# Kernel optimization log

Hardware: AMD Instinct MI355X
Metric: run time of the kernel (lower is better)

The kernel has to match this reference:

```python
import jax, jax.numpy as jnp
import numpy as np

DIM = 2048
N_HEADS = 16
HEAD_DIM = 128
KV_HEADS = 1
ROPE_BASE = 10000.0


def _rope_tables(T, dim, dtype):
    inv_freq = 1.0 / (ROPE_BASE ** (jnp.arange(0, dim, 2, dtype=jnp.float32) / dim))
    t = jnp.arange(T, dtype=jnp.float32)
    freqs = jnp.einsum('i,j->ij', t, inv_freq)          # [T, dim/2]
    emb = jnp.concatenate([freqs, freqs], axis=-1)      # [T, dim]
    cos = jnp.cos(emb)[None, None, :, :].astype(dtype)  # [1,1,T,dim]
    sin = jnp.sin(emb)[None, None, :, :].astype(dtype)
    return cos, sin


def _rotate_half(x):
    x1, x2 = jnp.split(x, 2, axis=-1)
    return jnp.concatenate([-x2, x1], axis=-1)


def setup_inputs() -> dict:
    key = jax.random.key(0)
    k1, k2, k3, k4, k5 = jax.random.split(key, 5)
    B, T = 2, 2048
    x = jax.random.normal(k1, (B, T, DIM), dtype=jnp.float32)
    # additive causal mask: 0 on/below diagonal, -1e9 above
    causal = jnp.triu(jnp.full((T, T), -1e9, dtype=jnp.float32), k=1)
    attn_mask = causal[None, None, :, :]
    s = 1.0 / np.sqrt(DIM)
    wq = jax.random.normal(k2, (DIM, N_HEADS * HEAD_DIM), dtype=jnp.float32) * s
    wk = jax.random.normal(k3, (DIM, KV_HEADS * HEAD_DIM), dtype=jnp.float32) * s
    wv = jax.random.normal(k4, (DIM, KV_HEADS * HEAD_DIM), dtype=jnp.float32) * s
    wo = jax.random.normal(k5, (N_HEADS * HEAD_DIM, DIM), dtype=jnp.float32) * s
    return {"x": x, "attn_mask": attn_mask, "wq": wq, "wk": wk, "wv": wv, "wo": wo}


def reference(x, attn_mask, wq, wk, wv, wo):
    B, T, C = x.shape
    q = (x @ wq).reshape(B, T, N_HEADS, HEAD_DIM).transpose(0, 2, 1, 3)   # [B,H,T,d]
    k = (x @ wk).reshape(B, T, KV_HEADS, HEAD_DIM).transpose(0, 2, 1, 3)  # [B,1,T,d]
    v = (x @ wv).reshape(B, T, KV_HEADS, HEAD_DIM).transpose(0, 2, 1, 3)  # [B,1,T,d]
    cos, sin = _rope_tables(T, HEAD_DIM, x.dtype)
    q = q * cos + _rotate_half(q) * sin
    k = k * cos + _rotate_half(k) * sin
    # KV head broadcasts over the H dim inside matmul (MQA expand path)
    att = jnp.matmul(q, k.swapaxes(-1, -2)) / np.sqrt(HEAD_DIM)          # [B,H,T,T]
    att = att + attn_mask
    w = jax.nn.softmax(att, axis=-1)
    y = jnp.matmul(w, v)                                                  # [B,H,T,d]
    y = y.transpose(0, 2, 1, 3).reshape(B, T, N_HEADS * HEAD_DIM)
    y = y @ wo
    k_exp = jnp.broadcast_to(k, (B, N_HEADS, T, HEAD_DIM))
    v_exp = jnp.broadcast_to(v, (B, N_HEADS, T, HEAD_DIM))
    return y, k_exp, v_exp
```

## Files before the change

kernel.cpp:

```cpp
#include <hip/hip_runtime.h>
#include <hip/hip_bf16.h>
#include <cstdint>
#include <cstddef>

#define B_SZ   2
#define T_SEQ  2048
#define C_DIM  2048
#define NH     16
#define HD     128

typedef __attribute__((ext_vector_type(8))) short s8v;
typedef __attribute__((ext_vector_type(4))) float f32x4;

typedef __attribute__((address_space(3))) char lds_char;
typedef __attribute__((address_space(1))) const char glob_char;

__device__ __forceinline__ unsigned short f2bf(float f) {
    union { float f; uint32_t i; } v; v.f = f;
    uint32_t r = (v.i + 0x7FFFu + ((v.i >> 16) & 1u)) >> 16;
    return (unsigned short)r;
}

__device__ __forceinline__ unsigned short cvt1_bf16(float f) {
    unsigned int w;
    asm("v_cvt_pk_bf16_f32 %0, %1, %2" : "=v"(w) : "v"(f), "v"(f));
    return (unsigned short)w;
}

template <int CTRL>
__device__ __forceinline__ float dpp_ror_f(float x) {
    int t = __builtin_amdgcn_update_dpp(__float_as_int(x), __float_as_int(x),
                                        CTRL, 0xf, 0xf, false);
    return __int_as_float(t);
}
__device__ __forceinline__ float rowmax16(float v) {
    v = fmaxf(v, dpp_ror_f<0x121>(v));
    v = fmaxf(v, dpp_ror_f<0x122>(v));
    v = fmaxf(v, dpp_ror_f<0x124>(v));
    v = fmaxf(v, dpp_ror_f<0x128>(v));
    return v;
}

__global__ void k_f32_to_bf16(const float* __restrict__ in,
                              unsigned short* __restrict__ out, int n4) {
    int i = blockIdx.x * blockDim.x + threadIdx.x;
    int stride = gridDim.x * blockDim.x;
    for (; i < n4; i += stride) {
        float4 v = reinterpret_cast<const float4*>(in)[i];
        ushort4 o;
        o.x = f2bf(v.x); o.y = f2bf(v.y); o.z = f2bf(v.z); o.w = f2bf(v.w);
        reinterpret_cast<ushort4*>(out)[i] = o;
    }
}

__global__ void k_transp_bf16(const float* __restrict__ in,
                              unsigned short* __restrict__ out,
                              int R, int C, int ldo) {
    __shared__ unsigned short tile[64][66];
    int x0 = blockIdx.x * 64, y0 = blockIdx.y * 64;
    int tx = threadIdx.x, ty = threadIdx.y;
#pragma unroll
    for (int j = 0; j < 16; ++j) {
        int r = y0 + ty + j * 4;
        tile[ty + j * 4][tx] = f2bf(in[(size_t)r * C + x0 + tx]);
    }
    __syncthreads();
#pragma unroll
    for (int j = 0; j < 16; ++j) {
        int orow = x0 + ty + j * 4;
        out[(size_t)orow * ldo + y0 + tx] = tile[tx][ty + j * 4];
    }
}

__global__ void k_rope_tab(float* __restrict__ cosT, float* __restrict__ sinT) {
    int idx = blockIdx.x * blockDim.x + threadIdx.x;
    if (idx >= T_SEQ * 64) return;
    int t = idx >> 6, i = idx & 63;
    float inv = powf(10000.0f, -(float)i / 64.0f);
    float ang = (float)t * inv;
    cosT[idx] = cosf(ang);
    sinT[idx] = sinf(ang);
}

#define BM 128
#define BN 128
#define BK 64

__global__ __launch_bounds__(256) void k_gemm_bt(
        const unsigned short* __restrict__ A,
        const unsigned short* __restrict__ Bt,
        float* __restrict__ C, int M, int N, int K, int ldc) {
    __shared__ char smem[BM * BK * 2 + BN * BK * 2];
    char* As = smem;
    char* Bs = smem + BM * BK * 2;
    int tid = threadIdx.x, lane = tid & 63, wid = tid >> 6;
    int m0 = blockIdx.y * BM, n0 = blockIdx.x * BN;
    int wr = wid >> 1, wc = wid & 1;

    f32x4 acc[4][4] = {};

    int srow = wid * 32 + (lane >> 3);
    int cp = lane & 7;

    for (int k0 = 0; k0 < K; k0 += BK) {
#pragma unroll
        for (int i = 0; i < 4; ++i) {
            int row = srow + i * 8;
            int c = cp ^ (row & 7);
            const unsigned short* ga = A + (size_t)(m0 + row) * K + k0 + c * 8;
            const unsigned short* gb = Bt + (size_t)(n0 + row) * K + k0 + c * 8;
            __builtin_amdgcn_global_load_lds((glob_char*)ga,
                (lds_char*)(As + wid * 4096 + i * 1024), 16, 0, 0);
            __builtin_amdgcn_global_load_lds((glob_char*)gb,
                (lds_char*)(Bs + wid * 4096 + i * 1024), 16, 0, 0);
        }
        __syncthreads();

#pragma unroll
        for (int kc = 0; kc < 2; ++kc) {
            s8v af[4], bfr[4];
#pragma unroll
            for (int mi = 0; mi < 4; ++mi) {
                int row = wr * 64 + mi * 16 + (lane & 15);
                int slot = (kc * 4 + (lane >> 4)) ^ (row & 7);
                af[mi] = *reinterpret_cast<const s8v*>(As + row * 128 + slot * 16);
            }
#pragma unroll
            for (int ni = 0; ni < 4; ++ni) {
                int row = wc * 64 + ni * 16 + (lane & 15);
                int slot = (kc * 4 + (lane >> 4)) ^ (row & 7);
                bfr[ni] = *reinterpret_cast<const s8v*>(Bs + row * 128 + slot * 16);
            }
#pragma unroll
            for (int mi = 0; mi < 4; ++mi)
#pragma unroll
                for (int ni = 0; ni < 4; ++ni)
                    acc[mi][ni] = __builtin_amdgcn_mfma_f32_16x16x32_bf16(
                        af[mi], bfr[ni], acc[mi][ni], 0, 0, 0);
        }
        __syncthreads();
    }

#pragma unroll
    for (int mi = 0; mi < 4; ++mi) {
        int row = m0 + wr * 64 + mi * 16 + ((lane >> 4) << 2);
#pragma unroll
        for (int ni = 0; ni < 4; ++ni) {
            int col = n0 + wc * 64 + ni * 16 + (lane & 15);
            float* cp2 = C + (size_t)row * ldc + col;
#pragma unroll
            for (int r = 0; r < 4; ++r)
                cp2[(size_t)r * ldc] = acc[mi][ni][r];
        }
    }
}

__global__ void k_qkv_transform(const float* __restrict__ qkv,
                                const float* __restrict__ cosT,
                                const float* __restrict__ sinT,
                                unsigned short* __restrict__ qB,
                                unsigned short* __restrict__ kB,
                                unsigned short* __restrict__ vT,
                                float* __restrict__ kexp,
                                float* __restrict__ vexp) {
    int bt = blockIdx.x;
    int b = bt >> 11, t = bt & 2047;
    int tid = threadIdx.x;
    const float* base = qkv + (size_t)bt * 2304;
    const float SCALE = 0.08838834764831845f * 1.4426950408889634f;

    for (int i = tid; i < 1024; i += 256) {
        int h = i >> 6, d = i & 63;
        float c = cosT[t * 64 + d], s = sinT[t * 64 + d];
        float q1 = base[h * 128 + d], q2 = base[h * 128 + d + 64];
        float o1 = (q1 * c - q2 * s) * SCALE;
        float o2 = (q2 * c + q1 * s) * SCALE;
        size_t qoff = ((size_t)(b * NH + h) * T_SEQ + t) * HD + d;
        qB[qoff] = f2bf(o1);
        qB[qoff + 64] = f2bf(o2);
    }
    if (tid < 64) {
        int d = tid;
        float c = cosT[t * 64 + d], s = sinT[t * 64 + d];
        float k1 = base[2048 + d], k2 = base[2048 + d + 64];
        float o1 = k1 * c - k2 * s;
        float o2 = k2 * c + k1 * s;
        size_t koff = ((size_t)b * T_SEQ + t) * HD + d;
        kB[koff] = f2bf(o1);
        kB[koff + 64] = f2bf(o2);
#pragma unroll
        for (int h = 0; h < NH; ++h) {
            size_t eoff = ((size_t)(b * NH + h) * T_SEQ + t) * HD + d;
            kexp[eoff] = o1;
            kexp[eoff + 64] = o2;
        }
    }
    if (tid >= 128) {
        int d = tid - 128;
        float v = base[2176 + d];
        vT[((size_t)b * HD + d) * T_SEQ + t] = f2bf(v);
#pragma unroll
        for (int h = 0; h < NH; ++h)
            vexp[((size_t)(b * NH + h) * T_SEQ + t) * HD + d] = v;
    }
}

__global__ __launch_bounds__(256, 2) void k_flash_attn(
        const unsigned short* __restrict__ qB,
        const unsigned short* __restrict__ kB,
        const unsigned short* __restrict__ vT,
        unsigned short* __restrict__ yattn) {
    __shared__ char smem[81920];
    int tid = threadIdx.x, lane = tid & 63, wvid = tid >> 6;
    int blk = blockIdx.x;
    int g = blk >> 5;
    int qt = (g < 8) ? (15 - 2 * g) : (2 * g - 16);
    int bh = blk & 31;
    int b = bh >> 4, h = bh & 15;
    int q0 = qt * 128 + wvid * 32;

    char* Ks0 = smem;
    char* Vs0 = smem + 32768;
    char* pbase = smem + 65536 + wvid * 4096;

    const unsigned short* kbB   = kB + (size_t)b * T_SEQ * HD;
    const unsigned short* vbase = vT + (size_t)b * HD * T_SEQ;

    const unsigned short* qbase = qB + ((size_t)(b * NH + h) * T_SEQ + q0) * HD;
    s8v aq[2][4];
#pragma unroll
    for (int rt = 0; rt < 2; ++rt)
#pragma unroll
        for (int kc = 0; kc < 4; ++kc) {
            int row = rt * 16 + (lane & 15);
            aq[rt][kc] = *reinterpret_cast<const s8v*>(
                qbase + (size_t)row * HD + kc * 32 + (lane >> 4) * 8);
        }

    float m_r[2][4], l_r[2][4];
#pragma unroll
    for (int rt = 0; rt < 2; ++rt)
#pragma unroll
        for (int r = 0; r < 4; ++r) { m_r[rt][r] = -3e38f; l_r[rt][r] = 0.f; }
    f32x4 o[2][8] = {};

    int NT = 2 * qt + 2;

    auto stage = [&](int buf, int t) {
        int kv0 = t * 64;
#pragma unroll
        for (int j = 0; j < 4; ++j) {
            int n = j * 256 + tid;
            int row = n >> 4, ch = n & 15;
            const unsigned short* src =
                kbB + (size_t)(kv0 + row) * HD + (ch ^ (row & 7)) * 8;
            __builtin_amdgcn_global_load_lds((glob_char*)src,
                (lds_char*)(Ks0 + buf * 16384 + j * 4096 + wvid * 1024), 16, 0, 0);
        }
#pragma unroll
        for (int j = 0; j < 4; ++j) {
            int n = j * 256 + tid;
            int row = n >> 3, ch = n & 7;
            const unsigned short* src =
                vbase + (size_t)row * T_SEQ + kv0 + (ch ^ (row & 7)) * 8;
            __builtin_amdgcn_global_load_lds((glob_char*)src,
                (lds_char*)(Vs0 + buf * 16384 + j * 4096 + wvid * 1024), 16, 0, 0);
        }
    };

    stage(0, 0);
    asm volatile("s_waitcnt vmcnt(0)" ::: "memory");
    __builtin_amdgcn_s_barrier();
    __builtin_amdgcn_sched_barrier(0);

    for (int t = 0; t < NT; ++t) {
        int cur = t & 1;
        if (t + 1 < NT) stage(cur ^ 1, t + 1);
        int kv0 = t * 64;
        const char* Kc = Ks0 + cur * 16384;
        const char* Vc = Vs0 + cur * 16384;

        f32x4 sfr[2][4] = {};
        __builtin_amdgcn_s_setprio(1);
#pragma unroll
        for (int kc = 0; kc < 4; ++kc) {
            s8v kf[4];
#pragma unroll
            for (int n = 0; n < 4; ++n) {
                int row = n * 16 + (lane & 15);
                int byte = row * 256 +
                    ((kc * 64 + (lane >> 4) * 16) ^ ((row & 7) << 4));
                kf[n] = *reinterpret_cast<const s8v*>(Kc + byte);
            }
#pragma unroll
            for (int rt = 0; rt < 2; ++rt)
#pragma unroll
                for (int n = 0; n < 4; ++n)
                    sfr[rt][n] = __builtin_amdgcn_mfma_f32_16x16x32_bf16(
                        aq[rt][kc], kf[n], sfr[rt][n], 0, 0, 0);
        }
        __builtin_amdgcn_s_setprio(0);

        if (kv0 + 63 > q0) {
#pragma unroll
            for (int rt = 0; rt < 2; ++rt)
#pragma unroll
                for (int n = 0; n < 4; ++n)
#pragma unroll
                    for (int r = 0; r < 4; ++r) {
                        int col = kv0 + n * 16 + (lane & 15);
                        int row = q0 + rt * 16 + ((lane >> 4) << 2) + r;
                        if (col > row) sfr[rt][n][r] = -1e9f;
                    }
        }

#pragma unroll
        for (int rt = 0; rt < 2; ++rt) {
            float pm[4];
#pragma unroll
            for (int r = 0; r < 4; ++r) {
                float v0 = fmaxf(fmaxf(sfr[rt][0][r], sfr[rt][1][r]),
                                 fmaxf(sfr[rt][2][r], sfr[rt][3][r]));
                pm[r] = rowmax16(v0);
            }
            int ok = (pm[0] <= m_r[rt][0] + 8.0f) &
                     (pm[1] <= m_r[rt][1] + 8.0f) &
                     (pm[2] <= m_r[rt][2] + 8.0f) &
                     (pm[3] <= m_r[rt][3] + 8.0f);
            if (!__all(ok)) {
#pragma unroll
                for (int r = 0; r < 4; ++r) {
                    float mn = fmaxf(m_r[rt][r], pm[r]);
                    float al = exp2f(m_r[rt][r] - mn);
                    l_r[rt][r] *= al;
#pragma unroll
                    for (int ds = 0; ds < 8; ++ds)
                        o[rt][ds][r] *= al;
                    m_r[rt][r] = mn;
                }
            }
#pragma unroll
            for (int n = 0; n < 4; ++n)
#pragma unroll
                for (int r = 0; r < 4; ++r) {
                    float p = exp2f(sfr[rt][n][r] - m_r[rt][r]);
                    sfr[rt][n][r] = p;
                    l_r[rt][r] += p;
                }
        }

#pragma unroll
        for (int rt = 0; rt < 2; ++rt)
#pragma unroll
            for (int n = 0; n < 4; ++n)
#pragma unroll
                for (int r = 0; r < 4; ++r) {
                    int rowl = rt * 16 + ((lane >> 4) << 2) + r;
                    int byte = rowl * 128 + (n * 16 + (lane & 15)) * 2;
                    byte ^= ((rowl & 7) << 4);
                    *reinterpret_cast<unsigned short*>(pbase + byte) =
                        cvt1_bf16(sfr[rt][n][r]);
                }
        asm volatile("s_waitcnt lgkmcnt(0)" ::: "memory");
        __builtin_amdgcn_sched_barrier(0);

        __builtin_amdgcn_s_setprio(1);
#pragma unroll
        for (int kc2 = 0; kc2 < 2; ++kc2) {
            s8v pa[2];
#pragma unroll
            for (int rt = 0; rt < 2; ++rt) {
                int rowl = rt * 16 + (lane & 15);
                int byte = rowl * 128 +
                    ((kc2 * 64 + (lane >> 4) * 16) ^ ((rowl & 7) << 4));
                pa[rt] = *reinterpret_cast<const s8v*>(pbase + byte);
            }
#pragma unroll
            for (int ds = 0; ds < 8; ++ds) {
                int vrow = ds * 16 + (lane & 15);
                int vbyte = vrow * 128 +
                    ((kc2 * 64 + (lane >> 4) * 16) ^ ((vrow & 7) << 4));
                s8v bv = *reinterpret_cast<const s8v*>(Vc + vbyte);
#pragma unroll
                for (int rt = 0; rt < 2; ++rt)
                    o[rt][ds] = __builtin_amdgcn_mfma_f32_16x16x32_bf16(
                        pa[rt], bv, o[rt][ds], 0, 0, 0);
            }
        }
        __builtin_amdgcn_s_setprio(0);

        asm volatile("s_waitcnt vmcnt(0) lgkmcnt(0)" ::: "memory");
        __builtin_amdgcn_s_barrier();
        __builtin_amdgcn_sched_barrier(0);
    }

#pragma unroll
    for (int rt = 0; rt < 2; ++rt) {
        float inv[4];
#pragma unroll
        for (int r = 0; r < 4; ++r) {
            float lv = l_r[rt][r];
#pragma unroll
            for (int off = 1; off < 16; off <<= 1)
                lv += __shfl_xor(lv, off);
            inv[r] = 1.0f / lv;
        }
#pragma unroll
        for (int ds = 0; ds < 8; ++ds)
#pragma unroll
            for (int r = 0; r < 4; ++r) {
                int row = q0 + rt * 16 + ((lane >> 4) << 2) + r;
                int col = h * HD + ds * 16 + (lane & 15);
                yattn[((size_t)b * T_SEQ + row) * C_DIM + col] =
                    cvt1_bf16(o[rt][ds][r] * inv[r]);
            }
    }
}

extern "C" void kernel_launch(void* const* d_in, const int* in_sizes, int n_in,
                              void* d_out, int out_size, void* d_ws, size_t ws_size,
                              hipStream_t stream) {
    const float* x  = (const float*)d_in[0];
    const float* wq = (const float*)d_in[2];
    const float* wk = (const float*)d_in[3];
    const float* wv = (const float*)d_in[4];
    const float* wo = (const float*)d_in[5];

    char* ws = (char*)d_ws;
    size_t off = 0;
    auto alloc = [&](size_t bytes) -> void* {
        void* p = ws + off;
        off += (bytes + 255) & ~(size_t)255;
        return p;
    };
    unsigned short* xb   = (unsigned short*)alloc((size_t)4096 * 2048 * 2);
    unsigned short* wT   = (unsigned short*)alloc((size_t)2304 * 2048 * 2);
    unsigned short* woT  = (unsigned short*)alloc((size_t)2048 * 2048 * 2);
    float*          qkv  = (float*)alloc((size_t)4096 * 2304 * 4);
    float*          cosT = (float*)alloc((size_t)2048 * 64 * 4);
    float*          sinT = (float*)alloc((size_t)2048 * 64 * 4);
    unsigned short* qB   = (unsigned short*)alloc((size_t)2 * 16 * 2048 * 128 * 2);
    unsigned short* kB   = (unsigned short*)alloc((size_t)2 * 2048 * 128 * 2);
    unsigned short* vT   = (unsigned short*)alloc((size_t)2 * 128 * 2048 * 2);
    unsigned short* yattn = (unsigned short*)qkv;

    float* y_out = (float*)d_out;
    float* kexp  = y_out + (size_t)2 * 2048 * 2048;
    float* vexp  = kexp + (size_t)2 * 16 * 2048 * 128;

    dim3 tb(64, 4);
    k_f32_to_bf16<<<2048, 256, 0, stream>>>(x, xb, 4096 * 2048 / 4);
    k_transp_bf16<<<dim3(32, 32), tb, 0, stream>>>(wq, wT, 2048, 2048, 2048);
    k_transp_bf16<<<dim3(2, 32), tb, 0, stream>>>(wk, wT + (size_t)2048 * 2048, 2048, 128, 2048);
    k_transp_bf16<<<dim3(2, 32), tb, 0, stream>>>(wv, wT + (size_t)2176 * 2048, 2048, 128, 2048);
    k_transp_bf16<<<dim3(32, 32), tb, 0, stream>>>(wo, woT, 2048, 2048, 2048);
    k_rope_tab<<<512, 256, 0, stream>>>(cosT, sinT);

    k_gemm_bt<<<dim3(2304 / BN, 4096 / BM), 256, 0, stream>>>(
        xb, wT, qkv, 4096, 2304, 2048, 2304);
    k_qkv_transform<<<4096, 256, 0, stream>>>(qkv, cosT, sinT, qB, kB, vT, kexp, vexp);
    k_flash_attn<<<512, 256, 0, stream>>>(qB, kB, vT, yattn);
    k_gemm_bt<<<dim3(2048 / BN, 4096 / BM), 256, 0, stream>>>(
        yattn, woT, y_out, 4096, 2048, 2048, 2048);
}
```

Before: 253.8 us.

## Pair mirrored 64-row query tiles per block for balanced causal attention work

Measured after the change: 252.5 us. No clear change (-0.5%).

```diff
diff --git a/kernel.cpp b/kernel.cpp
--- a/kernel.cpp
+++ b/kernel.cpp
@@ -213,11 +213,15 @@
     __shared__ char smem[81920];
     int tid = threadIdx.x, lane = tid & 63, wvid = tid >> 6;
     int blk = blockIdx.x;
-    int g = blk >> 5;
-    int qt = (g < 8) ? (15 - 2 * g) : (2 * g - 16);
-    int bh = blk & 31;
-    int b = bh >> 4, h = bh & 15;
-    int q0 = qt * 128 + wvid * 32;
+    int b = blk >> 8;
+    int rem = blk & 255;
+    int h = rem & 15;
+    int jj = rem >> 4;
+    int j0 = 16 + jj;
+    int j1 = 15 - jj;
+    int qrow0[2];
+    qrow0[0] = j0 * 64 + wvid * 16;
+    qrow0[1] = j1 * 64 + wvid * 16;
 
     char* Ks0 = smem;
     char* Vs0 = smem + 32768;
@@ -226,16 +230,16 @@
     const unsigned short* kbB   = kB + (size_t)b * T_SEQ * HD;
     const unsigned short* vbase = vT + (size_t)b * HD * T_SEQ;
 
-    const unsigned short* qbase = qB + ((size_t)(b * NH + h) * T_SEQ + q0) * HD;
     s8v aq[2][4];
 #pragma unroll
-    for (int rt = 0; rt < 2; ++rt)
-#pragma unroll
-        for (int kc = 0; kc < 4; ++kc) {
-            int row = rt * 16 + (lane & 15);
+    for (int rt = 0; rt < 2; ++rt) {
+        const unsigned short* qbase =
+            qB + ((size_t)(b * NH + h) * T_SEQ + qrow0[rt]) * HD;
+#pragma unroll
+        for (int kc = 0; kc < 4; ++kc)
             aq[rt][kc] = *reinterpret_cast<const s8v*>(
-                qbase + (size_t)row * HD + kc * 32 + (lane >> 4) * 8);
-        }
+                qbase + (size_t)(lane & 15) * HD + kc * 32 + (lane >> 4) * 8);
+    }
 
     float m_r[2][4], l_r[2][4];
 #pragma unroll
@@ -244,7 +248,7 @@
         for (int r = 0; r < 4; ++r) { m_r[rt][r] = -3e38f; l_r[rt][r] = 0.f; }
     f32x4 o[2][8] = {};
 
-    int NT = 2 * qt + 2;
+    int NT = j0 + 1;
 
     auto stage = [&](int buf, int t) {
         int kv0 = t * 64;
@@ -279,6 +283,7 @@
         int kv0 = t * 64;
         const char* Kc = Ks0 + cur * 16384;
         const char* Vc = Vs0 + cur * 16384;
+        int act1 = (t <= j1);
 
         f32x4 sfr[2][4] = {};
         __builtin_amdgcn_s_setprio(1);
@@ -293,29 +298,31 @@
                 kf[n] = *reinterpret_cast<const s8v*>(Kc + byte);
             }
 #pragma unroll
-            for (int rt = 0; rt < 2; ++rt)
+            for (int n = 0; n < 4; ++n)
+                sfr[0][n] = __builtin_amdgcn_mfma_f32_16x16x32_bf16(
+                    aq[0][kc], kf[n], sfr[0][n], 0, 0, 0);
+            if (act1) {
 #pragma unroll
                 for (int n = 0; n < 4; ++n)
-                    sfr[rt][n] = __builtin_amdgcn_mfma_f32_16x16x32_bf16(
-                        aq[rt][kc], kf[n], sfr[rt][n], 0, 0, 0);
+                    sfr[1][n] = __builtin_amdgcn_mfma_f32_16x16x32_bf16(
+                        aq[1][kc], kf[n], sfr[1][n], 0, 0, 0);
+            }
         }
         __builtin_amdgcn_s_setprio(0);
 
-        if (kv0 + 63 > q0) {
-#pragma unroll
-            for (int rt = 0; rt < 2; ++rt)
+#pragma unroll
+        for (int rt = 0; rt < 2; ++rt) {
+            if (rt == 1 && !act1) continue;
+            if (kv0 + 63 > qrow0[rt]) {
 #pragma unroll
                 for (int n = 0; n < 4; ++n)
 #pragma unroll
                     for (int r = 0; r < 4; ++r) {
                         int col = kv0 + n * 16 + (lane & 15);
-                        int row = q0 + rt * 16 + ((lane >> 4) << 2) + r;
+                        int row = qrow0[rt] + ((lane >> 4) << 2) + r;
                         if (col > row) sfr[rt][n][r] = -1e9f;
                     }
-        }
-
-#pragma unroll
-        for (int rt = 0; rt < 2; ++rt) {
+            }
             float pm[4];
 #pragma unroll
             for (int r = 0; r < 4; ++r) {
@@ -350,7 +357,8 @@
         }
 
 #pragma unroll
-        for (int rt = 0; rt < 2; ++rt)
+        for (int rt = 0; rt < 2; ++rt) {
+            if (rt == 1 && !act1) continue;
 #pragma unroll
             for (int n = 0; n < 4; ++n)
 #pragma unroll
@@ -361,6 +369,7 @@
                     *reinterpret_cast<unsigned short*>(pbase + byte) =
                         cvt1_bf16(sfr[rt][n][r]);
                 }
+        }
         asm volatile("s_waitcnt lgkmcnt(0)" ::: "memory");
         __builtin_amdgcn_sched_barrier(0);
 
@@ -381,10 +390,11 @@
                 int vbyte = vrow * 128 +
                     ((kc2 * 64 + (lane >> 4) * 16) ^ ((vrow & 7) << 4));
                 s8v bv = *reinterpret_cast<const s8v*>(Vc + vbyte);
-#pragma unroll
-                for (int rt = 0; rt < 2; ++rt)
-                    o[rt][ds] = __builtin_amdgcn_mfma_f32_16x16x32_bf16(
-                        pa[rt], bv, o[rt][ds], 0, 0, 0);
+                o[0][ds] = __builtin_amdgcn_mfma_f32_16x16x32_bf16(
+                    pa[0], bv, o[0][ds], 0, 0, 0);
+                if (act1)
+                    o[1][ds] = __builtin_amdgcn_mfma_f32_16x16x32_bf16(
+                        pa[1], bv, o[1][ds], 0, 0, 0);
             }
         }
         __builtin_amdgcn_s_setprio(0);
@@ -409,7 +419,7 @@
         for (int ds = 0; ds < 8; ++ds)
 #pragma unroll
             for (int r = 0; r < 4; ++r) {
-                int row = q0 + rt * 16 + ((lane >> 4) << 2) + r;
+                int row = qrow0[rt] + ((lane >> 4) << 2) + r;
                 int col = h * HD + ds * 16 + (lane & 15);
                 yattn[((size_t)b * T_SEQ + row) * C_DIM + col] =
                     cvt1_bf16(o[rt][ds][r] * inv[r]);
```
